# Kernel tuning notes

Hardware: AMD Instinct MI355X
Metric: run time of the kernel (lower is better)

The kernel has to match this reference:

```python
import jax, jax.numpy as jnp
import numpy as np

N_DIM = 768
HIDDEN_DIM = 768
BATCH = 4
SEQ = 2048


def setup_inputs() -> dict:
    key = jax.random.key(0)
    ks = jax.random.split(key, 9)
    s_in = 1.0 / np.sqrt(N_DIM)
    s_h = 1.0 / np.sqrt(HIDDEN_DIM)
    return {
        "x": jax.random.normal(ks[0], (BATCH, SEQ, N_DIM), dtype=jnp.float32),
        # torch Linear weights: [out_features, in_features]
        "wq": jax.random.uniform(ks[1], (HIDDEN_DIM, N_DIM), jnp.float32, -s_in, s_in),
        "bq": jax.random.uniform(ks[2], (HIDDEN_DIM,), jnp.float32, -s_in, s_in),
        "wk": jax.random.uniform(ks[3], (HIDDEN_DIM, N_DIM), jnp.float32, -s_in, s_in),
        "bk": jax.random.uniform(ks[4], (HIDDEN_DIM,), jnp.float32, -s_in, s_in),
        "wv": jax.random.uniform(ks[5], (HIDDEN_DIM, N_DIM), jnp.float32, -s_in, s_in),
        "bv": jax.random.uniform(ks[6], (HIDDEN_DIM,), jnp.float32, -s_in, s_in),
        "wo": jax.random.uniform(ks[7], (N_DIM, HIDDEN_DIM), jnp.float32, -s_h, s_h),
        "bo": jax.random.uniform(ks[8], (N_DIM,), jnp.float32, -s_h, s_h),
    }


def reference(x, wq, bq, wk, bk, wv, bv, wo, bo):
    # q,k,v: [B, S, H]
    q = jnp.einsum("bsd,hd->bsh", x, wq) + bq
    k = jnp.einsum("bsd,hd->bsh", x, wk) + bk
    v = jnp.einsum("bsd,hd->bsh", x, wv) + bv
    # NOTE: faithful to source — no 1/sqrt(d) scaling, no mask.
    scores = jnp.einsum("bqh,bkh->bqk", q, k)  # [B, S, S]
    attn = jax.nn.softmax(scores, axis=-1)
    y = jnp.einsum("bqk,bkh->bqh", attn, v)  # [B, S, H]
    out = jnp.einsum("bsh,dh->bsd", y, wo) + bo
    return out
```

## Files before the change

kernel.cpp:

```cpp
#include <hip/hip_runtime.h>

typedef _Float16 f16;
typedef _Float16 f16x8 __attribute__((ext_vector_type(8)));
typedef float f32x4 __attribute__((ext_vector_type(4)));

#define GLD16(g, l) __builtin_amdgcn_global_load_lds( \
    (const __attribute__((address_space(1))) void*)(g), \
    (__attribute__((address_space(3))) void*)(l), 16, 0, 0)

template <typename OutT, int BM, int BN, int MODE>
__global__ __launch_bounds__(256, 4)
void gemm_kernel(const f16* __restrict__ A, long sA,
                 const f16* __restrict__ B, long sB,
                 void* __restrict__ Cv, long sC,
                 void* __restrict__ C2v,
                 const float* __restrict__ bias,
                 const float* __restrict__ bias2,
                 int N, int K)
{
    constexpr int FM = BM / 32;
    constexpr int FN = BN / 32;
    constexpr int IA = BM / 64;
    constexpr int IB = BN / 64;
    constexpr int RA = BM / 4;
    constexpr int RB = BN / 4;

    OutT* C  = (OutT*)Cv;
    OutT* C2 = (OutT*)C2v;
    const int tid  = threadIdx.x;
    const int wave = tid >> 6;
    const int lane = tid & 63;
    const int bz   = blockIdx.z;
    A += (long)bz * sA;
    B += (long)bz * sB;
    C += (long)bz * sC;
    const long bm = (long)blockIdx.x * BM;
    const long bn = (long)blockIdx.y * BN;

    __shared__ f16 sAt[BM * 32];
    __shared__ f16 sBt[BN * 32];

    const int srow = lane >> 2;
    const int sc   = lane & 3;
    const int gch  = (sc ^ ((srow >> 1) & 3)) * 8;

    const f16* gA[IA]; const f16* gB[IB];
    f16* lA[IA]; f16* lB[IB];
    #pragma unroll
    for (int i = 0; i < IA; ++i) {
        gA[i] = A + (bm + wave * RA + i * 16 + srow) * (long)K + gch;
        lA[i] = &sAt[(wave * RA + i * 16) * 32];
    }
    #pragma unroll
    for (int i = 0; i < IB; ++i) {
        gB[i] = B + (bn + wave * RB + i * 16 + srow) * (long)K + gch;
        lB[i] = &sBt[(wave * RB + i * 16) * 32];
    }

    const int wm = (wave >> 1) * (BM / 2);
    const int wn = (wave & 1) * (BN / 2);
    const int lr = lane & 15;
    const int qd = lane >> 4;
    const int swz = (qd ^ ((lr >> 1) & 3)) * 8;

    f32x4 acc[FM][FN] = {};

    for (int k0 = 0; k0 < K; k0 += 32) {
        #pragma unroll
        for (int i = 0; i < IA; ++i) { GLD16(gA[i], lA[i]); gA[i] += 32; }
        #pragma unroll
        for (int i = 0; i < IB; ++i) { GLD16(gB[i], lB[i]); gB[i] += 32; }
        __syncthreads();

        f16x8 af[FM], bf[FN];
        #pragma unroll
        for (int t = 0; t < FM; ++t)
            af[t] = *(const f16x8*)&sAt[(wm + t * 16 + lr) * 32 + swz];
        #pragma unroll
        for (int t = 0; t < FN; ++t)
            bf[t] = *(const f16x8*)&sBt[(wn + t * 16 + lr) * 32 + swz];
        #pragma unroll
        for (int tm = 0; tm < FM; ++tm)
            #pragma unroll
            for (int tn = 0; tn < FN; ++tn)
                acc[tm][tn] = __builtin_amdgcn_mfma_f32_16x16x32_f16(
                    af[tm], bf[tn], acc[tm][tn], 0, 0, 0);
        __syncthreads();
    }

    #pragma unroll
    for (int tn = 0; tn < FN; ++tn) {
        const long col = bn + wn + tn * 16 + lr;
        OutT* dst = C;
        long cc = col, stride = N;
        float bc = 0.f;
        if (MODE == 1) bc = bias[col];
        if (MODE == 3) {
            stride = 768;
            if (col >= 768) { dst = C2; cc = col - 768; bc = bias2[cc]; }
            else            { bc = bias[cc]; }
        }
        #pragma unroll
        for (int tm = 0; tm < FM; ++tm) {
            #pragma unroll
            for (int r = 0; r < 4; ++r) {
                const long row = bm + wm + tm * 16 + qd * 4 + r;
                float v = acc[tm][tn][r] + bc;
                if (MODE == 2) v += bias[row];
                dst[row * stride + cc] = (OutT)v;
            }
        }
    }
}

__global__ __launch_bounds__(256)
void softmax_kernel(f16* __restrict__ S)
{
    const long row = blockIdx.x;
    f16* p = S + row * 2048;
    const int tid  = threadIdx.x;
    const int wave = tid >> 6;
    const int lane = tid & 63;

    f16x8 x = *(const f16x8*)&p[tid * 8];
    float v[8];
    float m = -1e30f;
    #pragma unroll
    for (int j = 0; j < 8; ++j) { v[j] = (float)x[j]; m = fmaxf(m, v[j]); }
    #pragma unroll
    for (int off = 32; off > 0; off >>= 1) m = fmaxf(m, __shfl_down(m, off));

    __shared__ float rm[4], rs[4];
    if (lane == 0) rm[wave] = m;
    __syncthreads();
    m = fmaxf(fmaxf(rm[0], rm[1]), fmaxf(rm[2], rm[3]));

    float s = 0.f;
    #pragma unroll
    for (int j = 0; j < 8; ++j) { v[j] = __expf(v[j] - m); s += v[j]; }
    #pragma unroll
    for (int off = 32; off > 0; off >>= 1) s += __shfl_down(s, off);
    if (lane == 0) rs[wave] = s;
    __syncthreads();
    s = rs[0] + rs[1] + rs[2] + rs[3];
    const float inv = 1.0f / s;

    f16x8 y;
    #pragma unroll
    for (int j = 0; j < 8; ++j) y[j] = (f16)(v[j] * inv);
    *(f16x8*)&p[tid * 8] = y;
}

__global__ __launch_bounds__(256)
void cvt_kernel(const float* __restrict__ in, f16* __restrict__ out)
{
    const long i = ((long)blockIdx.x * 256 + threadIdx.x) * 8;
    float4 a = *(const float4*)(in + i);
    float4 b = *(const float4*)(in + i + 4);
    f16x8 o;
    o[0] = (f16)a.x; o[1] = (f16)a.y; o[2] = (f16)a.z; o[3] = (f16)a.w;
    o[4] = (f16)b.x; o[5] = (f16)b.y; o[6] = (f16)b.z; o[7] = (f16)b.w;
    *(f16x8*)&out[i] = o;
}

__global__ __launch_bounds__(256)
void cvt4_kernel(const float* __restrict__ w0, const float* __restrict__ w1,
                 const float* __restrict__ w2, const float* __restrict__ w3,
                 f16* __restrict__ out)
{
    const int sel = blockIdx.y;
    const float* in = (sel == 0) ? w0 : (sel == 1) ? w1 : (sel == 2) ? w2 : w3;
    f16* o = out + (long)sel * 589824;
    const long i = ((long)blockIdx.x * 256 + threadIdx.x) * 8;
    float4 a = *(const float4*)(in + i);
    float4 b = *(const float4*)(in + i + 4);
    f16x8 v;
    v[0] = (f16)a.x; v[1] = (f16)a.y; v[2] = (f16)a.z; v[3] = (f16)a.w;
    v[4] = (f16)b.x; v[5] = (f16)b.y; v[6] = (f16)b.z; v[7] = (f16)b.w;
    *(f16x8*)&o[i] = v;
}

extern "C" void kernel_launch(void* const* d_in, const int* in_sizes, int n_in,
                              void* d_out, int out_size, void* d_ws, size_t ws_size,
                              hipStream_t stream)
{
    const float* x  = (const float*)d_in[0];
    const float* wq = (const float*)d_in[1];
    const float* bq = (const float*)d_in[2];
    const float* wk = (const float*)d_in[3];
    const float* bk = (const float*)d_in[4];
    const float* wv = (const float*)d_in[5];
    const float* bv = (const float*)d_in[6];
    const float* wo = (const float*)d_in[7];
    const float* bo = (const float*)d_in[8];

    char* ws = (char*)d_ws;
    f16* x16 = (f16*)(ws + 0);
    f16* w16 = (f16*)(ws + 12582912);
    f16* Q   = (f16*)(ws + 17301504);
    f16* Kb  = (f16*)(ws + 29884416);
    f16* VT  = (f16*)(ws + 42467328);
    f16* S   = (f16*)(ws + 55050240);
    f16* Y   = (f16*)(ws + 88604672);

    f16* wv16 = w16 + 2 * 589824;
    f16* wo16 = w16 + 3 * 589824;

    cvt_kernel<<<3072, 256, 0, stream>>>(x, x16);
    cvt4_kernel<<<dim3(288, 4), 256, 0, stream>>>(wq, wk, wv, wo, w16);

    gemm_kernel<f16, 128, 128, 3><<<dim3(64, 12, 1), 256, 0, stream>>>(
        x16, 0, w16, 0, Q, 0, Kb, bq, bk, 1536, 768);
    gemm_kernel<f16, 64, 128, 2><<<dim3(12, 16, 4), 256, 0, stream>>>(
        wv16, 0, x16, (long)2048 * 768, VT, (long)768 * 2048, nullptr,
        bv, nullptr, 2048, 768);
    gemm_kernel<f16, 128, 128, 0><<<dim3(16, 16, 4), 256, 0, stream>>>(
        Q, (long)2048 * 768, Kb, (long)2048 * 768, S, (long)2048 * 2048,
        nullptr, nullptr, nullptr, 2048, 768);
    softmax_kernel<<<8192, 256, 0, stream>>>(S);
    gemm_kernel<f16, 128, 64, 0><<<dim3(16, 12, 4), 256, 0, stream>>>(
        S, (long)2048 * 2048, VT, (long)768 * 2048, Y, (long)2048 * 768,
        nullptr, nullptr, nullptr, 768, 2048);
    gemm_kernel<float, 128, 64, 1><<<dim3(64, 12, 1), 256, 0, stream>>>(
        Y, 0, wo16, 0, (float*)d_out, 0, nullptr, bo, nullptr, 768, 768);
}
```

Before: 264.6 us.

## Fuse softmax into PV GEMM with online row stats and exp-on-load

Removes the standalone softmax pass over the score matrix. A new PV kernel first computes per-row max and sum with an online reduction over S, then applies exp on the fly to the S tiles loaded into shared memory before the MFMA, and scales by 1/sum in the epilogue. The scores GEMM moves to a dedicated kernel with a larger 128x256 tile. In exchange, S is read twice inside the PV kernel, the grid shrinks to 256 blocks, and exp work is duplicated across the two column blocks.

```diff
diff --git a/kernel.cpp b/kernel.cpp
--- a/kernel.cpp
+++ b/kernel.cpp
@@ -113,42 +113,191 @@
     }
 }
 
-__global__ __launch_bounds__(256)
-void softmax_kernel(f16* __restrict__ S)
-{
-    const long row = blockIdx.x;
-    f16* p = S + row * 2048;
+__global__ __launch_bounds__(256, 2)
+void scores_kernel(const f16* __restrict__ Q, const f16* __restrict__ Km,
+                   f16* __restrict__ S)
+{
     const int tid  = threadIdx.x;
     const int wave = tid >> 6;
     const int lane = tid & 63;
-
-    f16x8 x = *(const f16x8*)&p[tid * 8];
-    float v[8];
-    float m = -1e30f;
-    #pragma unroll
-    for (int j = 0; j < 8; ++j) { v[j] = (float)x[j]; m = fmaxf(m, v[j]); }
-    #pragma unroll
-    for (int off = 32; off > 0; off >>= 1) m = fmaxf(m, __shfl_down(m, off));
-
-    __shared__ float rm[4], rs[4];
-    if (lane == 0) rm[wave] = m;
+    const int bz   = blockIdx.z;
+    Q  += (long)bz * 2048 * 768;
+    Km += (long)bz * 2048 * 768;
+    S  += (long)bz * 2048 * 2048;
+    const long bm = (long)blockIdx.x * 128;
+    const long bn = (long)blockIdx.y * 256;
+
+    __shared__ f16 sA[128 * 32];
+    __shared__ f16 sB[256 * 32];
+
+    const int srow = lane >> 2;
+    const int sc   = lane & 3;
+    const int gch  = (sc ^ ((srow >> 1) & 3)) * 8;
+
+    const f16* gA0 = Q + (bm + wave * 32 + srow) * 768 + gch;
+    const f16* gA1 = gA0 + 16 * 768;
+    f16* lA0 = &sA[(wave * 32) * 32];
+    f16* lA1 = &sA[(wave * 32 + 16) * 32];
+    const f16* gB[4]; f16* lB[4];
+    #pragma unroll
+    for (int i = 0; i < 4; ++i) {
+        gB[i] = Km + (bn + wave * 64 + i * 16 + srow) * 768 + gch;
+        lB[i] = &sB[(wave * 64 + i * 16) * 32];
+    }
+
+    const int wm = (wave >> 1) * 64;
+    const int wn = (wave & 1) * 128;
+    const int lr = lane & 15;
+    const int qd = lane >> 4;
+    const int swz = (qd ^ ((lr >> 1) & 3)) * 8;
+
+    f32x4 acc[4][8] = {};
+
+    for (int s = 0; s < 24; ++s) {
+        const int ko = s * 32;
+        GLD16(gA0 + ko, lA0); GLD16(gA1 + ko, lA1);
+        #pragma unroll
+        for (int i = 0; i < 4; ++i) GLD16(gB[i] + ko, lB[i]);
+        __syncthreads();
+
+        f16x8 af[4], bf[8];
+        #pragma unroll
+        for (int t = 0; t < 4; ++t)
+            af[t] = *(const f16x8*)&sA[(wm + t * 16 + lr) * 32 + swz];
+        #pragma unroll
+        for (int t = 0; t < 8; ++t)
+            bf[t] = *(const f16x8*)&sB[(wn + t * 16 + lr) * 32 + swz];
+        #pragma unroll
+        for (int tm = 0; tm < 4; ++tm)
+            #pragma unroll
+            for (int tn = 0; tn < 8; ++tn)
+                acc[tm][tn] = __builtin_amdgcn_mfma_f32_16x16x32_f16(
+                    af[tm], bf[tn], acc[tm][tn], 0, 0, 0);
+        __syncthreads();
+    }
+
+    #pragma unroll
+    for (int tn = 0; tn < 8; ++tn) {
+        const long col = bn + wn + tn * 16 + lr;
+        #pragma unroll
+        for (int tm = 0; tm < 4; ++tm)
+            #pragma unroll
+            for (int r = 0; r < 4; ++r) {
+                const long row = bm + wm + tm * 16 + qd * 4 + r;
+                S[row * 2048 + col] = (f16)acc[tm][tn][r];
+            }
+    }
+}
+
+__global__ __launch_bounds__(256, 2)
+void pv_kernel(const f16* __restrict__ S, const f16* __restrict__ VT,
+               f16* __restrict__ Y)
+{
+    const int tid  = threadIdx.x;
+    const int wave = tid >> 6;
+    const int lane = tid & 63;
+    const int bz   = blockIdx.z;
+    S  += (long)bz * 2048 * 2048;
+    VT += (long)bz * 768 * 2048;
+    Y  += (long)bz * 2048 * 768;
+    const long r0 = (long)blockIdx.x * 64;
+    const long c0 = (long)blockIdx.y * 384;
+
+    __shared__ f16 sS[64 * 32];
+    __shared__ f16 sV[384 * 32];
+    __shared__ float pm[256], pl[256];
+    __shared__ float fm[64], fl[64];
+
+    {
+        const int rowp = tid >> 2;
+        const f16* sp = S + (r0 + rowp) * 2048 + (tid & 3) * 8;
+        float m = -3.0e38f, l = 0.f;
+        for (int i = 0; i < 64; ++i) {
+            f16x8 x = *(const f16x8*)(sp + i * 32);
+            float v[8], mx = -3.0e38f;
+            #pragma unroll
+            for (int j = 0; j < 8; ++j) { v[j] = (float)x[j]; mx = fmaxf(mx, v[j]); }
+            if (mx > m) { l *= __expf(m - mx); m = mx; }
+            #pragma unroll
+            for (int j = 0; j < 8; ++j) l += __expf(v[j] - m);
+        }
+        pm[tid] = m; pl[tid] = l;
+    }
     __syncthreads();
-    m = fmaxf(fmaxf(rm[0], rm[1]), fmaxf(rm[2], rm[3]));
-
-    float s = 0.f;
-    #pragma unroll
-    for (int j = 0; j < 8; ++j) { v[j] = __expf(v[j] - m); s += v[j]; }
-    #pragma unroll
-    for (int off = 32; off > 0; off >>= 1) s += __shfl_down(s, off);
-    if (lane == 0) rs[wave] = s;
+    if (tid < 64) {
+        const int b = tid * 4;
+        float m = fmaxf(fmaxf(pm[b], pm[b+1]), fmaxf(pm[b+2], pm[b+3]));
+        float l = pl[b]   * __expf(pm[b]   - m) + pl[b+1] * __expf(pm[b+1] - m)
+                + pl[b+2] * __expf(pm[b+2] - m) + pl[b+3] * __expf(pm[b+3] - m);
+        fm[tid] = m; fl[tid] = 1.0f / l;
+    }
     __syncthreads();
-    s = rs[0] + rs[1] + rs[2] + rs[3];
-    const float inv = 1.0f / s;
-
-    f16x8 y;
-    #pragma unroll
-    for (int j = 0; j < 8; ++j) y[j] = (f16)(v[j] * inv);
-    *(f16x8*)&p[tid * 8] = y;
+
+    const int rg = wave >> 1;
+    const int cg = wave & 1;
+    const int srow = lane >> 2;
+    const int sc   = lane & 3;
+    const int gch  = (sc ^ ((srow >> 1) & 3)) * 8;
+
+    const f16* gS = S + (r0 + wave * 16 + srow) * 2048 + gch;
+    f16* lS = &sS[(wave * 16) * 32];
+    const f16* gV[6]; f16* lV[6];
+    #pragma unroll
+    for (int i = 0; i < 6; ++i) {
+        gV[i] = VT + (c0 + wave * 96 + i * 16 + srow) * 2048 + gch;
+        lV[i] = &sV[(wave * 96 + i * 16) * 32];
+    }
+
+    const int lr = lane & 15;
+    const int qd = lane >> 4;
+    const int swz = (qd ^ ((lr >> 1) & 3)) * 8;
+
+    const float mr0 = fm[rg * 32 + lr];
+    const float mr1 = fm[rg * 32 + 16 + lr];
+
+    f32x4 acc[2][12] = {};
+
+    for (int s = 0; s < 64; ++s) {
+        const int ko = s * 32;
+        GLD16(gS + ko, lS);
+        #pragma unroll
+        for (int i = 0; i < 6; ++i) GLD16(gV[i] + ko, lV[i]);
+        __syncthreads();
+
+        f16x8 af[2];
+        {
+            f16x8 a0 = *(const f16x8*)&sS[(rg * 32 + lr) * 32 + swz];
+            f16x8 a1 = *(const f16x8*)&sS[(rg * 32 + 16 + lr) * 32 + swz];
+            #pragma unroll
+            for (int j = 0; j < 8; ++j) {
+                af[0][j] = (f16)__expf((float)a0[j] - mr0);
+                af[1][j] = (f16)__expf((float)a1[j] - mr1);
+            }
+        }
+        f16x8 bf[12];
+        #pragma unroll
+        for (int t = 0; t < 12; ++t)
+            bf[t] = *(const f16x8*)&sV[(cg * 192 + t * 16 + lr) * 32 + swz];
+        #pragma unroll
+        for (int tm = 0; tm < 2; ++tm)
+            #pragma unroll
+            for (int tn = 0; tn < 12; ++tn)
+                acc[tm][tn] = __builtin_amdgcn_mfma_f32_16x16x32_f16(
+                    af[tm], bf[tn], acc[tm][tn], 0, 0, 0);
+        __syncthreads();
+    }
+
+    #pragma unroll
+    for (int tn = 0; tn < 12; ++tn) {
+        const long col = c0 + cg * 192 + tn * 16 + lr;
+        #pragma unroll
+        for (int tm = 0; tm < 2; ++tm)
+            #pragma unroll
+            for (int r = 0; r < 4; ++r) {
+                const int rl = rg * 32 + tm * 16 + qd * 4 + r;
+                Y[(r0 + rl) * 768 + col] = (f16)(acc[tm][tn][r] * fl[rl]);
+            }
+    }
 }
 
 __global__ __launch_bounds__(256)
@@ -214,13 +363,8 @@
     gemm_kernel<f16, 64, 128, 2><<<dim3(12, 16, 4), 256, 0, stream>>>(
         wv16, 0, x16, (long)2048 * 768, VT, (long)768 * 2048, nullptr,
         bv, nullptr, 2048, 768);
-    gemm_kernel<f16, 128, 128, 0><<<dim3(16, 16, 4), 256, 0, stream>>>(
-        Q, (long)2048 * 768, Kb, (long)2048 * 768, S, (long)2048 * 2048,
-        nullptr, nullptr, nullptr, 2048, 768);
-    softmax_kernel<<<8192, 256, 0, stream>>>(S);
-    gemm_kernel<f16, 128, 64, 0><<<dim3(16, 12, 4), 256, 0, stream>>>(
-        S, (long)2048 * 2048, VT, (long)768 * 2048, Y, (long)2048 * 768,
-        nullptr, nullptr, nullptr, 768, 2048);
+    scores_kernel<<<dim3(16, 8, 4), 256, 0, stream>>>(Q, Kb, S);
+    pv_kernel<<<dim3(32, 2, 4), 256, 0, stream>>>(S, VT, Y);
     gemm_kernel<float, 128, 64, 1><<<dim3(64, 12, 1), 256, 0, stream>>>(
         Y, 0, wo16, 0, (float*)d_out, 0, nullptr, bo, nullptr, 768, 768);
 }
```

Measured after the change: 283.1 us. 7.0% more time.

## Double GEMM K-step to 64 with new swizzle, widen QK^T tile, fuse converts

Applied to the files above, without the earlier changes.

Each GEMM main-loop iteration now stages 64 K-elements per tile, using an 8-way XOR swizzle, and runs two MFMA sub-steps per iteration. This halves the number of barrier pairs per K. The QK^T GEMM tile is widened to 128x256 with a per-launch occupancy hint, launch bounds are made a template parameter, and the two conversion kernels are merged into one launch. The larger shared-memory tiles and accumulators lower occupancy, and loads are still not overlapped with compute.

```diff
diff --git a/kernel.cpp b/kernel.cpp
--- a/kernel.cpp
+++ b/kernel.cpp
@@ -8,8 +8,8 @@
     (const __attribute__((address_space(1))) void*)(g), \
     (__attribute__((address_space(3))) void*)(l), 16, 0, 0)
 
-template <typename OutT, int BM, int BN, int MODE>
-__global__ __launch_bounds__(256, 4)
+template <typename OutT, int BM, int BN, int MODE, int MINW>
+__global__ __launch_bounds__(256, MINW)
 void gemm_kernel(const f16* __restrict__ A, long sA,
                  const f16* __restrict__ B, long sB,
                  void* __restrict__ Cv, long sC,
@@ -20,10 +20,8 @@
 {
     constexpr int FM = BM / 32;
     constexpr int FN = BN / 32;
-    constexpr int IA = BM / 64;
-    constexpr int IB = BN / 64;
-    constexpr int RA = BM / 4;
-    constexpr int RB = BN / 4;
+    constexpr int IA = BM / 32;
+    constexpr int IB = BN / 32;
 
     OutT* C  = (OutT*)Cv;
     OutT* C2 = (OutT*)C2v;
@@ -37,54 +35,50 @@
     const long bm = (long)blockIdx.x * BM;
     const long bn = (long)blockIdx.y * BN;
 
-    __shared__ f16 sAt[BM * 32];
-    __shared__ f16 sBt[BN * 32];
-
-    const int srow = lane >> 2;
-    const int sc   = lane & 3;
-    const int gch  = (sc ^ ((srow >> 1) & 3)) * 8;
-
-    const f16* gA[IA]; const f16* gB[IB];
-    f16* lA[IA]; f16* lB[IB];
-    #pragma unroll
-    for (int i = 0; i < IA; ++i) {
-        gA[i] = A + (bm + wave * RA + i * 16 + srow) * (long)K + gch;
-        lA[i] = &sAt[(wave * RA + i * 16) * 32];
-    }
-    #pragma unroll
-    for (int i = 0; i < IB; ++i) {
-        gB[i] = B + (bn + wave * RB + i * 16 + srow) * (long)K + gch;
-        lB[i] = &sBt[(wave * RB + i * 16) * 32];
-    }
+    __shared__ f16 sAt[BM * 64];
+    __shared__ f16 sBt[BN * 64];
+
+    const int srow = lane >> 3;
+    const int gch  = ((lane & 7) ^ srow) * 8;
+
+    const f16* gAb = A + (bm + wave * (BM / 4) + srow) * (long)K + gch;
+    const f16* gBb = B + (bn + wave * (BN / 4) + srow) * (long)K + gch;
 
     const int wm = (wave >> 1) * (BM / 2);
     const int wn = (wave & 1) * (BN / 2);
     const int lr = lane & 15;
     const int qd = lane >> 4;
-    const int swz = (qd ^ ((lr >> 1) & 3)) * 8;
+    const int swz0 = ((0 * 4 + qd) ^ (lr & 7)) * 8;
+    const int swz1 = ((1 * 4 + qd) ^ (lr & 7)) * 8;
 
     f32x4 acc[FM][FN] = {};
 
-    for (int k0 = 0; k0 < K; k0 += 32) {
-        #pragma unroll
-        for (int i = 0; i < IA; ++i) { GLD16(gA[i], lA[i]); gA[i] += 32; }
-        #pragma unroll
-        for (int i = 0; i < IB; ++i) { GLD16(gB[i], lB[i]); gB[i] += 32; }
+    for (int k0 = 0; k0 < K; k0 += 64) {
+        #pragma unroll
+        for (int i = 0; i < IA; ++i)
+            GLD16(gAb + k0 + (long)i * 8 * K, &sAt[(wave * (BM / 4) + i * 8) * 64]);
+        #pragma unroll
+        for (int i = 0; i < IB; ++i)
+            GLD16(gBb + k0 + (long)i * 8 * K, &sBt[(wave * (BN / 4) + i * 8) * 64]);
         __syncthreads();
 
-        f16x8 af[FM], bf[FN];
-        #pragma unroll
-        for (int t = 0; t < FM; ++t)
-            af[t] = *(const f16x8*)&sAt[(wm + t * 16 + lr) * 32 + swz];
-        #pragma unroll
-        for (int t = 0; t < FN; ++t)
-            bf[t] = *(const f16x8*)&sBt[(wn + t * 16 + lr) * 32 + swz];
-        #pragma unroll
-        for (int tm = 0; tm < FM; ++tm)
-            #pragma unroll
-            for (int tn = 0; tn < FN; ++tn)
-                acc[tm][tn] = __builtin_amdgcn_mfma_f32_16x16x32_f16(
-                    af[tm], bf[tn], acc[tm][tn], 0, 0, 0);
+        #pragma unroll
+        for (int h = 0; h < 2; ++h) {
+            const int swz = h ? swz1 : swz0;
+            f16x8 af[FM], bf[FN];
+            #pragma unroll
+            for (int t = 0; t < FM; ++t)
+                af[t] = *(const f16x8*)&sAt[(wm + t * 16 + lr) * 64 + swz];
+            #pragma unroll
+            for (int t = 0; t < FN; ++t)
+                bf[t] = *(const f16x8*)&sBt[(wn + t * 16 + lr) * 64 + swz];
+            #pragma unroll
+            for (int tm = 0; tm < FM; ++tm)
+                #pragma unroll
+                for (int tn = 0; tn < FN; ++tn)
+                    acc[tm][tn] = __builtin_amdgcn_mfma_f32_16x16x32_f16(
+                        af[tm], bf[tn], acc[tm][tn], 0, 0, 0);
+        }
         __syncthreads();
     }
 
@@ -152,32 +146,28 @@
 }
 
 __global__ __launch_bounds__(256)
-void cvt_kernel(const float* __restrict__ in, f16* __restrict__ out)
-{
-    const long i = ((long)blockIdx.x * 256 + threadIdx.x) * 8;
+void cvt_all_kernel(const float* __restrict__ x,
+                    const float* __restrict__ w0, const float* __restrict__ w1,
+                    const float* __restrict__ w2, const float* __restrict__ w3,
+                    f16* __restrict__ x16, f16* __restrict__ w16)
+{
+    const float* in; f16* out; long i;
+    if (blockIdx.x < 3072) {
+        in = x; out = x16;
+        i = ((long)blockIdx.x * 256 + threadIdx.x) * 8;
+    } else {
+        const int wb  = blockIdx.x - 3072;
+        const int sel = wb / 288;
+        in  = (sel == 0) ? w0 : (sel == 1) ? w1 : (sel == 2) ? w2 : w3;
+        out = w16 + (long)sel * 589824;
+        i = ((long)(wb - sel * 288) * 256 + threadIdx.x) * 8;
+    }
     float4 a = *(const float4*)(in + i);
     float4 b = *(const float4*)(in + i + 4);
     f16x8 o;
     o[0] = (f16)a.x; o[1] = (f16)a.y; o[2] = (f16)a.z; o[3] = (f16)a.w;
     o[4] = (f16)b.x; o[5] = (f16)b.y; o[6] = (f16)b.z; o[7] = (f16)b.w;
     *(f16x8*)&out[i] = o;
-}
-
-__global__ __launch_bounds__(256)
-void cvt4_kernel(const float* __restrict__ w0, const float* __restrict__ w1,
-                 const float* __restrict__ w2, const float* __restrict__ w3,
-                 f16* __restrict__ out)
-{
-    const int sel = blockIdx.y;
-    const float* in = (sel == 0) ? w0 : (sel == 1) ? w1 : (sel == 2) ? w2 : w3;
-    f16* o = out + (long)sel * 589824;
-    const long i = ((long)blockIdx.x * 256 + threadIdx.x) * 8;
-    float4 a = *(const float4*)(in + i);
-    float4 b = *(const float4*)(in + i + 4);
-    f16x8 v;
-    v[0] = (f16)a.x; v[1] = (f16)a.y; v[2] = (f16)a.z; v[3] = (f16)a.w;
-    v[4] = (f16)b.x; v[5] = (f16)b.y; v[6] = (f16)b.z; v[7] = (f16)b.w;
-    *(f16x8*)&o[i] = v;
 }
 
 extern "C" void kernel_launch(void* const* d_in, const int* in_sizes, int n_in,
@@ -206,21 +196,20 @@
     f16* wv16 = w16 + 2 * 589824;
     f16* wo16 = w16 + 3 * 589824;
 
-    cvt_kernel<<<3072, 256, 0, stream>>>(x, x16);
-    cvt4_kernel<<<dim3(288, 4), 256, 0, stream>>>(wq, wk, wv, wo, w16);
-
-    gemm_kernel<f16, 128, 128, 3><<<dim3(64, 12, 1), 256, 0, stream>>>(
+    cvt_all_kernel<<<4224, 256, 0, stream>>>(x, wq, wk, wv, wo, x16, w16);
+
+    gemm_kernel<f16, 128, 128, 3, 3><<<dim3(64, 12, 1), 256, 0, stream>>>(
         x16, 0, w16, 0, Q, 0, Kb, bq, bk, 1536, 768);
-    gemm_kernel<f16, 64, 128, 2><<<dim3(12, 16, 4), 256, 0, stream>>>(
+    gemm_kernel<f16, 64, 128, 2, 4><<<dim3(12, 16, 4), 256, 0, stream>>>(
         wv16, 0, x16, (long)2048 * 768, VT, (long)768 * 2048, nullptr,
         bv, nullptr, 2048, 768);
-    gemm_kernel<f16, 128, 128, 0><<<dim3(16, 16, 4), 256, 0, stream>>>(
+    gemm_kernel<f16, 128, 256, 0, 2><<<dim3(16, 8, 4), 256, 0, stream>>>(
         Q, (long)2048 * 768, Kb, (long)2048 * 768, S, (long)2048 * 2048,
         nullptr, nullptr, nullptr, 2048, 768);
     softmax_kernel<<<8192, 256, 0, stream>>>(S);
-    gemm_kernel<f16, 128, 64, 0><<<dim3(16, 12, 4), 256, 0, stream>>>(
+    gemm_kernel<f16, 128, 64, 0, 4><<<dim3(16, 12, 4), 256, 0, stream>>>(
         S, (long)2048 * 2048, VT, (long)768 * 2048, Y, (long)2048 * 768,
         nullptr, nullptr, nullptr, 768, 2048);
-    gemm_kernel<float, 128, 64, 1><<<dim3(64, 12, 1), 256, 0, stream>>>(
+    gemm_kernel<float, 128, 64, 1, 4><<<dim3(64, 12, 1), 256, 0, stream>>>(
         Y, 0, wo16, 0, (float*)d_out, 0, nullptr, bo, nullptr, 768, 768);
 }
```

After: 224.6 us. -15.1%, faster.
